# Optimization experiments

Measured on AMD Instinct MI355X. Metric: run time of the kernel, lower is better.

Reference implementation:

```python
import jax, jax.numpy as jnp
import numpy as np

N_NODES = 100000
N_EDGES = 1_600_000
N_ROIS = 400
HIDDEN = 128
N_GRAPHS = 512
OUT = 2


def setup_inputs() -> dict:
    key = jax.random.key(0)
    ks = jax.random.split(key, 7)
    x = jax.random.normal(ks[0], (N_NODES, N_ROIS), dtype=jnp.float32)
    edge_index = jax.random.randint(ks[1], (2, N_EDGES), 0, N_NODES, dtype=jnp.int32)
    # sorted graph-assignment vector; prepend arange so every graph id is non-empty
    rnd = jax.random.randint(ks[2], (N_NODES - N_GRAPHS,), 0, N_GRAPHS, dtype=jnp.int32)
    batch = jnp.sort(jnp.concatenate([jnp.arange(N_GRAPHS, dtype=jnp.int32), rnd]))
    W = jax.random.normal(ks[3], (N_ROIS, HIDDEN), dtype=jnp.float32) / np.float32(np.sqrt(N_ROIS))
    b = jnp.zeros((HIDDEN,), dtype=jnp.float32)
    lin_W = jax.random.normal(ks[4], (HIDDEN, OUT), dtype=jnp.float32) / np.float32(np.sqrt(HIDDEN))
    lin_b = jnp.zeros((OUT,), dtype=jnp.float32)
    return {"x": x, "edge_index": edge_index, "batch": batch,
            "W": W, "b": b, "lin_W": lin_W, "lin_b": lin_b}


def reference(x, edge_index, batch, W, b, lin_W, lin_b):
    N = x.shape[0]
    # GCNConv: add self-loops, symmetric normalization D^-1/2 (A+I) D^-1/2
    loops = jnp.arange(N, dtype=edge_index.dtype)
    row = jnp.concatenate([edge_index[0], loops])  # source
    col = jnp.concatenate([edge_index[1], loops])  # target
    deg = jax.ops.segment_sum(jnp.ones_like(col, dtype=x.dtype), col, num_segments=N)
    dinv = jnp.where(deg > 0, jax.lax.rsqrt(deg), 0.0)
    norm = dinv[row] * dinv[col]                   # [E+N]
    h = x @ W                                      # [N, H] transform before propagate
    msg = h[row] * norm[:, None]                   # [E+N, H]
    agg = jax.ops.segment_sum(msg, col, num_segments=N) + b
    act = jax.nn.relu(agg)                         # [N, H]
    # global max pool over graph ids (all segments guaranteed non-empty)
    pooled = jax.ops.segment_max(act, batch, num_segments=N_GRAPHS)  # [G, H]
    logits = pooled @ lin_W + lin_b                # [G, OUT]
    return logits, pooled
```

## Files before the change

kernel.cpp:

```cpp
#include <hip/hip_runtime.h>
#include <hip/hip_bf16.h>

#define N_NODES 100000
#define N_EDGES 1600000
#define N_ROIS  400
#define HID     128
#define N_GRAPHS 512
#define NOUT    2
#define NBUCK   391
#define BCAP    8192
#define ECH     4096
#define NPW     16
#define NBLK_BUCKET 391
#define NBLK_PREP   208
#define NBLK_GEMM   782

typedef __attribute__((ext_vector_type(8))) short short8;
typedef __attribute__((ext_vector_type(4))) float f32x4;

static __device__ __forceinline__ unsigned short f2bf(float f) {
  __hip_bfloat16 h = __float2bfloat16(f);
  unsigned short u;
  __builtin_memcpy(&u, &h, 2);
  return u;
}
static __device__ __forceinline__ float bf2f(unsigned short h) {
  return __uint_as_float(((unsigned)h) << 16);
}

__global__ __launch_bounds__(256) void prep_bucket_k(
    const int* __restrict__ row, const int* __restrict__ col,
    int* __restrict__ bcnt, unsigned int* __restrict__ pairs,
    const float* __restrict__ W, unsigned short* __restrict__ Wf,
    float* __restrict__ pooled0) {
  __shared__ int hist[NBUCK];
  __shared__ int lbase[NBUCK];
  __shared__ int adj[NBUCK];
  __shared__ unsigned int spk[ECH];
  __shared__ unsigned short sbk[ECH];
  __shared__ int sc[256];
  int t = threadIdx.x;
  if (blockIdx.x >= NBLK_BUCKET) {
    int idx = (blockIdx.x - NBLK_BUCKET) * 256 + t;
    if (idx < 13 * 8 * 64 * 8) {
      int u    = idx & 7;
      int lane = (idx >> 3) & 63;
      int nt   = (idx >> 9) & 7;
      int kk5  = idx >> 12;
      int n = nt * 16 + (lane & 15);
      int k = kk5 * 32 + (lane >> 4) * 8 + u;
      Wf[idx] = (k < N_ROIS) ? f2bf(W[k * HID + n]) : (unsigned short)0;
    }
    int z = idx * 2;
    if (z < N_GRAPHS * HID) {
      float2 zz = {0.f, 0.f};
      *(float2*)(pooled0 + z) = zz;
    }
    return;
  }
  for (int b = t; b < NBUCK; b += 256) hist[b] = 0;
  __syncthreads();
  int e0 = blockIdx.x * ECH;
  int mtot = min(ECH, N_EDGES - e0);
  unsigned int pk[16];
  int bk[16], rk[16];
#pragma unroll
  for (int i = 0; i < 16; ++i) {
    int e = e0 + t + i * 256;
    if (e < N_EDGES) {
      int r = row[e], c = col[e];
      bk[i] = c >> 8;
      pk[i] = ((unsigned)r << 8) | (unsigned)(c & 255);
      rk[i] = atomicAdd(&hist[bk[i]], 1);
    } else bk[i] = -1;
  }
  __syncthreads();
  int v0 = hist[t];
  sc[t] = v0;
  __syncthreads();
  for (int off = 1; off < 256; off <<= 1) {
    int v = (t >= off) ? sc[t - off] : 0;
    __syncthreads();
    sc[t] += v;
    __syncthreads();
  }
  lbase[t] = sc[t] - v0;
  int tot0 = sc[255];
  __syncthreads();
  int v1 = (t < NBUCK - 256) ? hist[256 + t] : 0;
  sc[t] = v1;
  __syncthreads();
  for (int off = 1; off < 256; off <<= 1) {
    int v = (t >= off) ? sc[t - off] : 0;
    __syncthreads();
    sc[t] += v;
    __syncthreads();
  }
  if (t < NBUCK - 256) lbase[256 + t] = tot0 + sc[t] - v1;
  __syncthreads();
#pragma unroll
  for (int i = 0; i < 16; ++i)
    if (bk[i] >= 0) {
      int pos = lbase[bk[i]] + rk[i];
      spk[pos] = pk[i];
      sbk[pos] = (unsigned short)bk[i];
    }
  for (int b = t; b < NBUCK; b += 256)
    adj[b] = (hist[b] > 0) ? atomicAdd(&bcnt[b], hist[b]) : 0;
  __syncthreads();
  for (int j = t; j < mtot; j += 256) {
    int b = sbk[j];
    int p = adj[b] + (j - lbase[b]);
    if (p < BCAP) pairs[(size_t)b * BCAP + p] = spk[j];
  }
}

__global__ __launch_bounds__(512, 4) void csr_gemm_k(
    const unsigned int* __restrict__ pairs, const int* __restrict__ bcnt,
    int* __restrict__ csr_row, int* __restrict__ offs, int* __restrict__ cnt,
    float* __restrict__ dinv,
    const float* __restrict__ x, const unsigned short* __restrict__ Wf,
    unsigned short* __restrict__ hp) {
  __shared__ __align__(16) struct {
    unsigned int ep[BCAP];
    int h[256]; int sc2[256]; int cur[256];
  } c;
  int t = threadIdx.x;

  if (blockIdx.x < NBUCK) {
    bool act = t < 256;
    int b = blockIdx.x;
    int m = min(bcnt[b], BCAP);
    size_t base = (size_t)b * BCAP;
    for (int j = t; j < m; j += 512) c.ep[j] = pairs[base + j];
    if (act) c.h[t] = 0;
    __syncthreads();
    for (int j = t; j < m; j += 512) atomicAdd(&c.h[c.ep[j] & 255u], 1);
    __syncthreads();
    int myc = act ? c.h[t] : 0;
    int mycp = (myc + 3) & ~3;
    if (act) c.sc2[t] = mycp;
    __syncthreads();
    for (int off = 1; off < 256; off <<= 1) {
      int v = (act && t >= off) ? c.sc2[t - off] : 0;
      __syncthreads();
      if (act) c.sc2[t] += v;
      __syncthreads();
    }
    if (act) {
      int loff = c.sc2[t] - mycp;
      c.cur[t] = loff;
      int node = b * 256 + t;
      if (node < N_NODES) {
        cnt[node] = myc;
        offs[node] = (int)base + loff;
        dinv[node] = rsqrtf((float)(myc + 1));
      }
    }
    __syncthreads();
    for (int j = t; j < m; j += 512) {
      unsigned int e = c.ep[j];
      int pos = atomicAdd(&c.cur[e & 255u], 1);
      if (pos < BCAP) csr_row[base + pos] = (int)(e >> 8);
    }
    return;
  }

  int lane = t & 63, wv = t >> 6;
  int mrow = lane & 15, kg = lane >> 4;
  int row0 = (blockIdx.x - NBUCK) * 128;
  int arow = row0 + wv * 16 + mrow;
  bool rowok = arow < N_NODES;
  const float* xp = x + (size_t)arow * N_ROIS;
  const short8* wp = (const short8*)Wf + lane;

  f32x4 acc[8];
#pragma unroll
  for (int i = 0; i < 8; ++i) acc[i] = (f32x4){0.f, 0.f, 0.f, 0.f};

#pragma unroll
  for (int kf = 0; kf < 13; ++kf) {
    int k0 = kf * 32 + kg * 8;
    short8 a8;
    if (rowok && k0 + 8 <= N_ROIS) {
      float4 f0 = *(const float4*)(xp + k0);
      float4 f1 = *(const float4*)(xp + k0 + 4);
      a8[0] = (short)f2bf(f0.x); a8[1] = (short)f2bf(f0.y);
      a8[2] = (short)f2bf(f0.z); a8[3] = (short)f2bf(f0.w);
      a8[4] = (short)f2bf(f1.x); a8[5] = (short)f2bf(f1.y);
      a8[6] = (short)f2bf(f1.z); a8[7] = (short)f2bf(f1.w);
    } else {
#pragma unroll
      for (int v = 0; v < 8; ++v) {
        int k = k0 + v;
        float f = (rowok && k < N_ROIS) ? xp[k] : 0.f;
        a8[v] = (short)f2bf(f);
      }
    }
#pragma unroll
    for (int nt = 0; nt < 8; ++nt) {
      short8 bf = wp[(kf * 8 + nt) * 64];
      acc[nt] = __builtin_amdgcn_mfma_f32_16x16x32_bf16(a8, bf, acc[nt], 0, 0, 0);
    }
  }

#pragma unroll
  for (int r = 0; r < 4; ++r) {
    int grow = row0 + wv * 16 + kg * 4 + r;
    if (grow < N_NODES) {
      unsigned short* op = hp + (size_t)grow * HID + mrow;
#pragma unroll
      for (int nt = 0; nt < 8; ++nt) op[nt * 16] = f2bf(acc[nt][r]);
    }
  }
}

static __device__ __forceinline__ void acc8s(float* a, uint4 u, float d) {
  a[0] = fmaf(d, bf2f((unsigned short)(u.x)), a[0]);
  a[1] = fmaf(d, bf2f((unsigned short)(u.x >> 16)), a[1]);
  a[2] = fmaf(d, bf2f((unsigned short)(u.y)), a[2]);
  a[3] = fmaf(d, bf2f((unsigned short)(u.y >> 16)), a[3]);
  a[4] = fmaf(d, bf2f((unsigned short)(u.z)), a[4]);
  a[5] = fmaf(d, bf2f((unsigned short)(u.z >> 16)), a[5]);
  a[6] = fmaf(d, bf2f((unsigned short)(u.w)), a[6]);
  a[7] = fmaf(d, bf2f((unsigned short)(u.w >> 16)), a[7]);
}

__global__ __launch_bounds__(256) void gather_k(
    const unsigned short* __restrict__ hp, const int* __restrict__ csr_row,
    const int* __restrict__ offs, const int* __restrict__ cnt,
    const float* __restrict__ dinv, const int* __restrict__ batch,
    const float* __restrict__ bias, unsigned int* __restrict__ pooled_bits) {
  int wave = (blockIdx.x * blockDim.x + threadIdx.x) >> 6;
  int lane = threadIdx.x & 63;
  int g  = lane >> 4;
  int cg = lane & 15;
  int n0 = wave * NPW;
  if (n0 >= N_NODES) return;
  int nend = min(n0 + NPW, N_NODES);
  float bv[8];
  {
    float4 b0 = *(const float4*)(bias + cg * 8);
    float4 b1 = *(const float4*)(bias + cg * 8 + 4);
    bv[0] = b0.x; bv[1] = b0.y; bv[2] = b0.z; bv[3] = b0.w;
    bv[4] = b1.x; bv[5] = b1.y; bv[6] = b1.z; bv[7] = b1.w;
  }
  float rm[8];
#pragma unroll
  for (int k = 0; k < 8; ++k) rm[k] = 0.f;
  int cur_g = batch[n0];

  for (int i = n0; i < nend; ++i) {
    int start = offs[i];
    int m = cnt[i];
    float di = dinv[i];
    float a[8];
#pragma unroll
    for (int k = 0; k < 8; ++k) a[k] = 0.f;
    if (g == 0) {
      uint4 u = *(const uint4*)(hp + (size_t)i * HID + cg * 8);
      acc8s(a, u, di);
    }
    for (int j = 0; j < m; j += 4) {
      int4 q = *(const int4*)(csr_row + start + j);
      int s = (g == 0) ? q.x : (g == 1) ? q.y : (g == 2) ? q.z : q.w;
      if (j + g < m) {
        float dv = dinv[s];
        uint4 u = *(const uint4*)(hp + (size_t)s * HID + cg * 8);
        acc8s(a, u, dv);
      }
    }
#pragma unroll
    for (int k = 0; k < 8; ++k) {
      a[k] += __shfl_xor(a[k], 16);
      a[k] += __shfl_xor(a[k], 32);
    }
    int gb = batch[i];
    if (gb != cur_g) {
      if (lane < 16) {
#pragma unroll
        for (int k = 0; k < 8; ++k)
          atomicMax(&pooled_bits[cur_g * HID + cg * 8 + k], __float_as_uint(rm[k]));
      }
#pragma unroll
      for (int k = 0; k < 8; ++k) rm[k] = 0.f;
      cur_g = gb;
    }
#pragma unroll
    for (int k = 0; k < 8; ++k)
      rm[k] = fmaxf(rm[k], fmaxf(fmaf(di, a[k], bv[k]), 0.f));
  }
  if (lane < 16) {
#pragma unroll
    for (int k = 0; k < 8; ++k)
      atomicMax(&pooled_bits[cur_g * HID + cg * 8 + k], __float_as_uint(rm[k]));
  }
}

__global__ void logits_k(const float* __restrict__ pooled, const float* __restrict__ lin_W,
                         const float* __restrict__ lin_b, float* __restrict__ out) {
  int t = blockIdx.x * blockDim.x + threadIdx.x;
  if (t < N_GRAPHS * NOUT) {
    int g = t >> 1, o = t & 1;
    float s = lin_b[o];
    const float* pg = pooled + g * HID;
#pragma unroll 8
    for (int k = 0; k < HID; ++k) s = fmaf(pg[k], lin_W[k * NOUT + o], s);
    out[t] = s;
  }
}

extern "C" void kernel_launch(void* const* d_in, const int* in_sizes, int n_in,
                              void* d_out, int out_size, void* d_ws, size_t ws_size,
                              hipStream_t stream) {
  (void)in_sizes; (void)n_in; (void)ws_size; (void)out_size;
  const float* x     = (const float*)d_in[0];
  const int*   ei    = (const int*)d_in[1];
  const int*   row   = ei;
  const int*   col   = ei + N_EDGES;
  const int*   batch = (const int*)d_in[2];
  const float* W     = (const float*)d_in[3];
  const float* b     = (const float*)d_in[4];
  const float* lin_W = (const float*)d_in[5];
  const float* lin_b = (const float*)d_in[6];
  float* out = (float*)d_out;
  float* pooled0 = out + N_GRAPHS * NOUT;

  char* ws = (char*)d_ws;
  int*   bcnt    = (int*)(ws + 0);
  int*   offs    = (int*)(ws + 4096);
  int*   cnt     = (int*)(ws + 404096);
  float* dinv    = (float*)(ws + 804096);
  unsigned short* Wf = (unsigned short*)(ws + 1204096);
  int*   csr_row = (int*)(ws + 1310720);
  unsigned int* pairs = (unsigned int*)(ws + 14123008);
  unsigned short* hp  = (unsigned short*)(ws + 26935296);

  hipMemsetAsync(bcnt, 0, NBUCK * sizeof(int), stream);

  prep_bucket_k<<<NBLK_BUCKET + NBLK_PREP, 256, 0, stream>>>(
      row, col, bcnt, pairs, W, Wf, pooled0);
  csr_gemm_k<<<NBUCK + NBLK_GEMM, 512, 0, stream>>>(
      pairs, bcnt, csr_row, offs, cnt, dinv, x, Wf, hp);
  {
    int waves = (N_NODES + NPW - 1) / NPW;
    int blocks = (waves * 64 + 255) / 256;
    gather_k<<<blocks, 256, 0, stream>>>(
        hp, csr_row, offs, cnt, dinv, batch, b,
        (unsigned int*)pooled0);
  }
  logits_k<<<(N_GRAPHS * NOUT + 255) / 256, 256, 0, stream>>>(
      pooled0, lin_W, lin_b, out);
}
```

Baseline: 404.9 us.

## Stage W fragments in LDS via global_load_lds for GEMM blocks

The GEMM half of csr_gemm_k now loads the pre-swizzled bf16 weight fragments into shared memory in four phases, using direct global-to-LDS loads. The bucket scratch and the W staging buffer share one union. Each wave then reads its B operands from LDS instead of from global memory or L2, which cuts repeated global traffic for W. Launch bounds go from 4 to 8 waves per SIMD to raise occupancy. The cost is extra barriers and vmcnt waits per phase, with no overlap between the W load and compute, plus more register pressure from the higher occupancy target.

```diff
diff --git a/kernel.cpp b/kernel.cpp
--- a/kernel.cpp
+++ b/kernel.cpp
@@ -26,6 +26,12 @@
 }
 static __device__ __forceinline__ float bf2f(unsigned short h) {
   return __uint_as_float(((unsigned)h) << 16);
+}
+
+static __device__ __forceinline__ void gload_lds16(const unsigned short* g, short* l) {
+  __builtin_amdgcn_global_load_lds(
+      (const __attribute__((address_space(1))) void*)g,
+      (__attribute__((address_space(3))) void*)l, 16, 0, 0);
 }
 
 __global__ __launch_bounds__(256) void prep_bucket_k(
@@ -115,16 +121,19 @@
   }
 }
 
-__global__ __launch_bounds__(512, 4) void csr_gemm_k(
+__global__ __launch_bounds__(512, 8) void csr_gemm_k(
     const unsigned int* __restrict__ pairs, const int* __restrict__ bcnt,
     int* __restrict__ csr_row, int* __restrict__ offs, int* __restrict__ cnt,
     float* __restrict__ dinv,
     const float* __restrict__ x, const unsigned short* __restrict__ Wf,
     unsigned short* __restrict__ hp) {
-  __shared__ __align__(16) struct {
-    unsigned int ep[BCAP];
-    int h[256]; int sc2[256]; int cur[256];
-  } c;
+  __shared__ __align__(16) union {
+    struct {
+      unsigned int ep[BCAP];
+      int h[256]; int sc2[256]; int cur[256];
+    } c;
+    short Bs[16384];
+  } u;
   int t = threadIdx.x;
 
   if (blockIdx.x < NBUCK) {
@@ -132,24 +141,24 @@
     int b = blockIdx.x;
     int m = min(bcnt[b], BCAP);
     size_t base = (size_t)b * BCAP;
-    for (int j = t; j < m; j += 512) c.ep[j] = pairs[base + j];
-    if (act) c.h[t] = 0;
-    __syncthreads();
-    for (int j = t; j < m; j += 512) atomicAdd(&c.h[c.ep[j] & 255u], 1);
-    __syncthreads();
-    int myc = act ? c.h[t] : 0;
+    for (int j = t; j < m; j += 512) u.c.ep[j] = pairs[base + j];
+    if (act) u.c.h[t] = 0;
+    __syncthreads();
+    for (int j = t; j < m; j += 512) atomicAdd(&u.c.h[u.c.ep[j] & 255u], 1);
+    __syncthreads();
+    int myc = act ? u.c.h[t] : 0;
     int mycp = (myc + 3) & ~3;
-    if (act) c.sc2[t] = mycp;
+    if (act) u.c.sc2[t] = mycp;
     __syncthreads();
     for (int off = 1; off < 256; off <<= 1) {
-      int v = (act && t >= off) ? c.sc2[t - off] : 0;
+      int v = (act && t >= off) ? u.c.sc2[t - off] : 0;
       __syncthreads();
-      if (act) c.sc2[t] += v;
+      if (act) u.c.sc2[t] += v;
       __syncthreads();
     }
     if (act) {
-      int loff = c.sc2[t] - mycp;
-      c.cur[t] = loff;
+      int loff = u.c.sc2[t] - mycp;
+      u.c.cur[t] = loff;
       int node = b * 256 + t;
       if (node < N_NODES) {
         cnt[node] = myc;
@@ -159,8 +168,8 @@
     }
     __syncthreads();
     for (int j = t; j < m; j += 512) {
-      unsigned int e = c.ep[j];
-      int pos = atomicAdd(&c.cur[e & 255u], 1);
+      unsigned int e = u.c.ep[j];
+      int pos = atomicAdd(&u.c.cur[e & 255u], 1);
       if (pos < BCAP) csr_row[base + pos] = (int)(e >> 8);
     }
     return;
@@ -172,36 +181,51 @@
   int arow = row0 + wv * 16 + mrow;
   bool rowok = arow < N_NODES;
   const float* xp = x + (size_t)arow * N_ROIS;
-  const short8* wp = (const short8*)Wf + lane;
 
   f32x4 acc[8];
 #pragma unroll
   for (int i = 0; i < 8; ++i) acc[i] = (f32x4){0.f, 0.f, 0.f, 0.f};
 
-#pragma unroll
-  for (int kf = 0; kf < 13; ++kf) {
-    int k0 = kf * 32 + kg * 8;
-    short8 a8;
-    if (rowok && k0 + 8 <= N_ROIS) {
-      float4 f0 = *(const float4*)(xp + k0);
-      float4 f1 = *(const float4*)(xp + k0 + 4);
-      a8[0] = (short)f2bf(f0.x); a8[1] = (short)f2bf(f0.y);
-      a8[2] = (short)f2bf(f0.z); a8[3] = (short)f2bf(f0.w);
-      a8[4] = (short)f2bf(f1.x); a8[5] = (short)f2bf(f1.y);
-      a8[6] = (short)f2bf(f1.z); a8[7] = (short)f2bf(f1.w);
-    } else {
-#pragma unroll
-      for (int v = 0; v < 8; ++v) {
-        int k = k0 + v;
-        float f = (rowok && k < N_ROIS) ? xp[k] : 0.f;
-        a8[v] = (short)f2bf(f);
-      }
-    }
-#pragma unroll
-    for (int nt = 0; nt < 8; ++nt) {
-      short8 bf = wp[(kf * 8 + nt) * 64];
-      acc[nt] = __builtin_amdgcn_mfma_f32_16x16x32_bf16(a8, bf, acc[nt], 0, 0, 0);
-    }
+  const int pk0[4] = {0, 4, 7, 10};
+  const int pnk[4] = {4, 3, 3, 3};
+
+#pragma unroll
+  for (int ph = 0; ph < 4; ++ph) {
+    int cbase = pk0[ph] * 8;
+#pragma unroll
+    for (int c = 0; c < pnk[ph]; ++c) {
+      int ch = wv * pnk[ph] + c;
+      gload_lds16(Wf + ((size_t)cbase + ch) * 512 + lane * 8, &u.Bs[ch * 512]);
+    }
+    asm volatile("s_waitcnt vmcnt(0)" ::: "memory");
+    __syncthreads();
+#pragma unroll
+    for (int kfl = 0; kfl < pnk[ph]; ++kfl) {
+      int kf = pk0[ph] + kfl;
+      int k0 = kf * 32 + kg * 8;
+      short8 a8;
+      if (rowok && k0 + 8 <= N_ROIS) {
+        float4 f0 = *(const float4*)(xp + k0);
+        float4 f1 = *(const float4*)(xp + k0 + 4);
+        a8[0] = (short)f2bf(f0.x); a8[1] = (short)f2bf(f0.y);
+        a8[2] = (short)f2bf(f0.z); a8[3] = (short)f2bf(f0.w);
+        a8[4] = (short)f2bf(f1.x); a8[5] = (short)f2bf(f1.y);
+        a8[6] = (short)f2bf(f1.z); a8[7] = (short)f2bf(f1.w);
+      } else {
+#pragma unroll
+        for (int v = 0; v < 8; ++v) {
+          int k = k0 + v;
+          float f = (rowok && k < N_ROIS) ? xp[k] : 0.f;
+          a8[v] = (short)f2bf(f);
+        }
+      }
+#pragma unroll
+      for (int nt = 0; nt < 8; ++nt) {
+        short8 bf = *(const short8*)&u.Bs[(kfl * 8 + nt) * 512 + lane * 8];
+        acc[nt] = __builtin_amdgcn_mfma_f32_16x16x32_bf16(a8, bf, acc[nt], 0, 0, 0);
+      }
+    }
+    __syncthreads();
   }
 
 #pragma unroll
```

Measured after the change: 390.0 us. 1.04x faster.
